# Optimization experiments

Hardware: AMD Instinct MI355X
Metric: run time of the kernel (lower is better)

Reference implementation:

```python
import jax, jax.numpy as jnp
import numpy as np

HEADS = 7
DIM_HEAD = 64
SCALE = DIM_HEAD ** -0.5


def setup_inputs() -> dict:
    key = jax.random.key(0)
    ks = jax.random.split(key, 6)
    b, n, dim = 8, 1024, 448
    inner = HEADS * DIM_HEAD  # 448
    x = jax.random.normal(ks[0], (b, n, dim), dtype=jnp.float32)
    w_qv = jax.random.normal(ks[1], (dim, 2 * inner), dtype=jnp.float32) * 0.02
    ext_k = jax.random.normal(ks[2], (HEADS, n, DIM_HEAD), dtype=jnp.float32)
    ext_bias = jax.random.normal(ks[3], (HEADS, n, n), dtype=jnp.float32)
    w_out = jax.random.normal(ks[4], (inner, dim), dtype=jnp.float32) * 0.02
    b_out = jnp.zeros((dim,), dtype=jnp.float32)
    return {"x": x, "w_qv": w_qv, "ext_k": ext_k, "ext_bias": ext_bias,
            "w_out": w_out, "b_out": b_out}


def reference(x, w_qv, ext_k, ext_bias, w_out, b_out):
    b, n, dim = x.shape
    qv = x @ w_qv                                   # [b, n, 2*inner]
    q, v = jnp.split(qv, 2, axis=-1)
    # b n (h d) -> b h n d
    q = q.reshape(b, n, HEADS, DIM_HEAD).transpose(0, 2, 1, 3)
    v = v.reshape(b, n, HEADS, DIM_HEAD).transpose(0, 2, 1, 3)
    # scores vs external learned key, additive bias applied BEFORE scale
    dots = (jnp.einsum('bhnd,hmd->bhnm', q, ext_k) + ext_bias[None]) * SCALE
    attn = jax.nn.softmax(dots, axis=-1)
    out = jnp.einsum('bhnm,bhmd->bhnd', attn, v)
    out = out.transpose(0, 2, 1, 3).reshape(b, n, HEADS * DIM_HEAD)
    return out @ w_out + b_out  # dropout is identity in eval mode
```

## Files before the change

kernel.cpp:

```cpp
#include <hip/hip_runtime.h>
#include <hip/hip_bf16.h>
#include <hip/hip_fp16.h>

#define BATCH 8
#define NSEQ 1024
#define DIMM 448
#define NHEAD 7
#define HDIM 64
#define MROWS (BATCH*NSEQ)
#define KDIM 448
#define SCALE_F 0.125f

typedef short short8 __attribute__((ext_vector_type(8)));
typedef float floatx16 __attribute__((ext_vector_type(16)));

#define MFMA32(a,b,c) __builtin_amdgcn_mfma_f32_32x32x16_bf16(a,b,c,0,0,0)

__device__ __forceinline__ unsigned short f2bf(float f){
    __hip_bfloat16 h = __float2bfloat16(f);
    return *reinterpret_cast<unsigned short*>(&h);
}
__device__ __forceinline__ float bf2f(unsigned short u){
    __hip_bfloat16 h; *reinterpret_cast<unsigned short*>(&h) = u;
    return __bfloat162float(h);
}
__device__ __forceinline__ float h2f(unsigned short u){
    __half h; *reinterpret_cast<unsigned short*>(&h) = u;
    return __half2float(h);
}
__device__ __forceinline__ unsigned short f2h(float f){
    __half h = __float2half(f);
    return *reinterpret_cast<unsigned short*>(&h);
}

__global__ __launch_bounds__(256)
void prep_all(const float* __restrict__ x, const float* __restrict__ ek,
              const float* __restrict__ wqv, const float* __restrict__ wout,
              const float* __restrict__ eb,
              unsigned short* __restrict__ xh, unsigned short* __restrict__ ekh,
              unsigned short* __restrict__ wqvTh, unsigned short* __restrict__ woTh,
              unsigned short* __restrict__ woTl, unsigned short* __restrict__ bp)
{
    __shared__ float T[2][64][33];
    const int bx = blockIdx.x, tid = threadIdx.x;

    if (bx < 3584) {
        int i = bx*256 + tid;
        float4 v = ((const float4*)x)[i];
        ((ushort4*)xh)[i] = make_ushort4(f2bf(v.x), f2bf(v.y), f2bf(v.z), f2bf(v.w));
    } else if (bx < 4032) {
        int i = (bx-3584)*256 + tid;
        float4 v = ((const float4*)ek)[i];
        ((ushort4*)ekh)[i] = make_ushort4(f2bf(v.x), f2bf(v.y), f2bf(v.z), f2bf(v.w));
    } else if (bx < 4228) {
        int lid = (bx-4032)*4 + (tid>>6);
        int kc = lid % 56, ng = lid / 56;
        int n = ng*64 + (tid&63);
        unsigned short h[8];
#pragma unroll
        for (int j = 0; j < 8; ++j) h[j] = f2bf(wqv[(size_t)(kc*8+j)*896 + n]);
        size_t o = (size_t)n*KDIM + kc*8;
        *(ushort4*)(wqvTh + o)     = make_ushort4(h[0],h[1],h[2],h[3]);
        *(ushort4*)(wqvTh + o + 4) = make_ushort4(h[4],h[5],h[6],h[7]);
    } else if (bx < 4340) {
        int lid = (bx-4228)*4 + (tid>>6);
        int kc = lid % 56, ng = lid / 56;
        int n = ng*64 + (tid&63);
        ushort4 h0={0,0,0,0}, h1={0,0,0,0}, l0={0,0,0,0}, l1={0,0,0,0};
        if (n < DIMM) {
            unsigned short h[8], l[8];
#pragma unroll
            for (int j = 0; j < 8; ++j) {
                float f = wout[(size_t)(kc*8+j)*DIMM + n];
                h[j] = f2bf(f); l[j] = f2bf(f - bf2f(h[j]));
            }
            h0 = make_ushort4(h[0],h[1],h[2],h[3]); h1 = make_ushort4(h[4],h[5],h[6],h[7]);
            l0 = make_ushort4(l[0],l[1],l[2],l[3]); l1 = make_ushort4(l[4],l[5],l[6],l[7]);
        }
        size_t o = (size_t)n*KDIM + kc*8;
        *(ushort4*)(woTh + o) = h0; *(ushort4*)(woTh + o + 4) = h1;
        *(ushort4*)(woTl + o) = l0; *(ushort4*)(woTl + o + 4) = l1;
    } else {
        const int sub = tid >> 7, st = tid & 127;
        const int lid = (bx-4340)*2 + sub;
        const int mt = lid & 31, qt = (lid>>5) & 15, h = lid >> 9;
#pragma unroll
        for (int it = 0; it < 4; ++it) {
            int idx = it*128 + st;
            int row = idx >> 3, c4 = (idx & 7)*4;
            float4 v = *(const float4*)(eb + ((size_t)(h*NSEQ + qt*64 + row))*NSEQ + mt*32 + c4);
            T[sub][row][c4+0]=v.x; T[sub][row][c4+1]=v.y;
            T[sub][row][c4+2]=v.z; T[sub][row][c4+3]=v.w;
        }
        __syncthreads();
        const int g2 = st >> 6, lane = st & 63;
        const int lq = lane & 31, quad = lane >> 5;
        const int q = g2*32 + lq;
        unsigned short* dst = bp + ((((size_t)h*16 + qt)*32 + mt)*4 + g2*2)*512 + lane*8;
#pragma unroll
        for (int jj = 0; jj < 2; ++jj) {
            unsigned short o[8];
#pragma unroll
            for (int t = 0; t < 8; ++t) {
                int m = (t&3) + 8*(t>>2) + 16*jj + 4*quad;
                o[t] = f2h(T[sub][q][m] * SCALE_F);
            }
            *(ushort4*)(dst + jj*512)     = make_ushort4(o[0],o[1],o[2],o[3]);
            *(ushort4*)(dst + jj*512 + 4) = make_ushort4(o[4],o[5],o[6],o[7]);
        }
    }
}

__global__ __launch_bounds__(256, 2)
void gemm1_grp(const unsigned short* __restrict__ Ah, const unsigned short* __restrict__ Bh,
               unsigned short* __restrict__ qd, unsigned short* __restrict__ vTd)
{
    const int tid = threadIdx.x;
    const int w = tid >> 6, lane = tid & 63;
    const int lq = lane & 31, lh = lane >> 5;
    const int m0 = (blockIdx.x*4 + w) * 64;
    const int y  = blockIdx.y;
    const int n0 = y * 64;
    const unsigned short* aB = Ah + (size_t)(m0 + lq)*KDIM + lh*8;
    const unsigned short* bB = Bh + (size_t)(n0 + lq)*KDIM + lh*8;

    floatx16 acc[2][2] = {};
    short8 aR[2][2][2], bR[2][2][2];
#define LD1(kt, par) {                                                        \
    _Pragma("unroll") for (int fm = 0; fm < 2; ++fm)                          \
    _Pragma("unroll") for (int c = 0; c < 2; ++c) {                           \
        aR[par][fm][c] = *(const short8*)(aB + (size_t)fm*32*KDIM + (kt)*32 + c*16); \
        bR[par][fm][c] = *(const short8*)(bB + (size_t)fm*32*KDIM + (kt)*32 + c*16); } }

    LD1(0, 0)
#pragma unroll
    for (int kt = 0; kt < 14; ++kt) {
        const int par = kt & 1;
        if (kt < 13) LD1(kt+1, par^1)
#pragma unroll
        for (int c = 0; c < 2; ++c)
#pragma unroll
            for (int fm = 0; fm < 2; ++fm)
#pragma unroll
                for (int fn = 0; fn < 2; ++fn)
                    acc[fm][fn] = MFMA32(aR[par][fm][c], bR[par][fn][c], acc[fm][fn]);
    }
#undef LD1

    if (y < NHEAD) {
#pragma unroll
        for (int fm = 0; fm < 2; ++fm)
#pragma unroll
            for (int fn = 0; fn < 2; ++fn) {
                const int d = fn*32 + lq;
#pragma unroll
                for (int r = 0; r < 16; ++r) {
                    const int gm = m0 + fm*32 + (r&3) + 8*(r>>2) + 4*lh;
                    const int b = gm >> 10, ns = gm & 1023;
                    qd[((size_t)((b*NHEAD + y)*NSEQ + ns))*HDIM + d] = f2bf(acc[fm][fn][r]);
                }
            }
    } else {
        const int head = y - NHEAD;
#pragma unroll
        for (int fm = 0; fm < 2; ++fm)
#pragma unroll
            for (int fn = 0; fn < 2; ++fn) {
                const int d = fn*32 + lq;
#pragma unroll
                for (int r = 0; r < 16; ++r) {
                    const int gm = m0 + fm*32 + (r&3) + 8*(r>>2) + 4*lh;
                    const int b = gm >> 10, ns = gm & 1023;
                    vTd[((size_t)((b*NHEAD + head)*HDIM + d))*NSEQ + ns] = f2bf(acc[fm][fn][r]);
                }
            }
    }
}

__global__ __launch_bounds__(256, 2)
void attn7s(const unsigned short* __restrict__ qh_g, const unsigned short* __restrict__ vTh,
            const unsigned short* __restrict__ ekh, const unsigned short* __restrict__ bp,
            unsigned short* __restrict__ aoh, unsigned short* __restrict__ aol)
{
    __shared__ unsigned short pS[4][1024];
    __shared__ float linv[4][2][32];

    const int tid = threadIdx.x;
    const int w = tid >> 6, lane = tid & 63;
    const int lq = lane & 31, lh = lane >> 5;

    const int orig = blockIdx.x;
    const int wg = (orig & 7)*28 + (orig >> 3);
    const int bq = wg & 1, qt = (wg >> 1) & 15, head = wg >> 5;
    const int b = bq*4 + w;
    const int bh = b*NHEAD + head;

    short8 qf[2][4];
#pragma unroll
    for (int g2 = 0; g2 < 2; ++g2)
#pragma unroll
        for (int c = 0; c < 4; ++c)
            qf[g2][c] = *(const short8*)(qh_g +
                ((size_t)(bh*NSEQ) + qt*64 + g2*32 + lq)*HDIM + c*16 + lh*8);

    const unsigned short* kB = ekh + ((size_t)head*NSEQ + lq)*HDIM + lh*8;
    const unsigned short* vB = vTh + ((size_t)(bh*HDIM) + lq)*NSEQ;
    const unsigned short* bB = bp + ((size_t)(head*16 + qt))*65536 + lane*8;

    short8 kR[2][4], vR[2][4], bR[2][4];
#define PREF(J, par) { const int mm = ((J) < 32) ? (J) : 0;                    \
    _Pragma("unroll") for (int c = 0; c < 4; ++c)                              \
        kR[par][c] = *(const short8*)(kB + (size_t)mm*2048 + c*16);            \
    _Pragma("unroll") for (int c2 = 0; c2 < 2; ++c2)                           \
    _Pragma("unroll") for (int h2 = 0; h2 < 2; ++h2)                           \
        vR[par][c2*2+h2] = *(const short8*)(vB + (size_t)(h2*32)*NSEQ + mm*32 + (c2*2+lh)*8); \
    _Pragma("unroll") for (int u = 0; u < 4; ++u)                              \
        bR[par][u] = *(const short8*)(bB + ((size_t)mm*4 + u)*512); }

    floatx16 O[2][2] = {};
    float ls[2] = {0.f, 0.f};

#define SEC(J, par, nxt) {                                                     \
    PREF((J)+1, nxt)                                                           \
    _Pragma("unroll") for (int g2 = 0; g2 < 2; ++g2) {                         \
        floatx16 S = {};                                                       \
        __builtin_amdgcn_s_setprio(1);                                         \
        _Pragma("unroll") for (int c = 0; c < 4; ++c)                          \
            S = MFMA32(kR[par][c], qf[g2][c], S);                              \
        __builtin_amdgcn_s_setprio(0);                                         \
        _Pragma("unroll") for (int g = 0; g < 4; ++g) {                        \
            unsigned short hb[4];                                              \
            _Pragma("unroll") for (int j2 = 0; j2 < 4; ++j2) {                 \
                const int i = g*4 + j2;                                        \
                float bs = h2f((unsigned short)bR[par][g2*2 + (i>>3)][i&7]);   \
                float pv = __expf(fmaf(S[i], SCALE_F, bs));                    \
                ls[g2] += pv;  hb[j2] = f2bf(pv);                              \
            }                                                                  \
            *(ushort4*)(pS[w] + g*256 + lq*8 + lh*4) = make_ushort4(hb[0],hb[1],hb[2],hb[3]); \
        }                                                                      \
        __builtin_amdgcn_s_setprio(1);                                         \
        _Pragma("unroll") for (int c2 = 0; c2 < 2; ++c2) {                     \
            short8 pf = *(const short8*)(pS[w] + ((c2*2+lh)*32 + lq)*8);       \
            O[g2][0] = MFMA32(pf, vR[par][c2*2+0], O[g2][0]);                  \
            O[g2][1] = MFMA32(pf, vR[par][c2*2+1], O[g2][1]);                  \
        }                                                                      \
        __builtin_amdgcn_s_setprio(0);                                         \
    } }

    PREF(0, 0)
    for (int jj = 0; jj < 16; ++jj) {
        SEC(2*jj,   0, 1)
        SEC(2*jj+1, 1, 0)
    }
#undef SEC
#undef PREF

    float lt0 = ls[0] + __shfl_xor(ls[0], 32);
    float lt1 = ls[1] + __shfl_xor(ls[1], 32);
    if (lh == 0) { linv[w][0][lq] = 1.f/lt0; linv[w][1][lq] = 1.f/lt1; }

#pragma unroll
    for (int g2 = 0; g2 < 2; ++g2)
#pragma unroll
        for (int r = 0; r < 16; ++r) {
            const int qr = (r&3) + 8*(r>>2) + 4*lh;
            const float inv = linv[w][g2][qr];
            const size_t o = ((size_t)(b*NSEQ) + qt*64 + g2*32 + qr)*DIMM + head*HDIM + lq;
            float v0 = O[g2][0][r]*inv, v1 = O[g2][1][r]*inv;
            unsigned short h0 = f2bf(v0), h1 = f2bf(v1);
            aoh[o]      = h0;  aol[o]      = f2bf(v0 - bf2f(h0));
            aoh[o + 32] = h1;  aol[o + 32] = f2bf(v1 - bf2f(h1));
        }
}

__global__ __launch_bounds__(128, 2)
void gemm2_grp(const unsigned short* __restrict__ Ah, const unsigned short* __restrict__ Al,
               const unsigned short* __restrict__ Bh, const unsigned short* __restrict__ Bl,
               const float* __restrict__ bias, float* __restrict__ out)
{
    const int tid = threadIdx.x;
    const int w = tid >> 6, lane = tid & 63;
    const int lq = lane & 31, lh = lane >> 5;
    const int m0 = (blockIdx.x*2 + w) * 64;
    const int n0 = blockIdx.y * 64;
    const unsigned short* aBh = Ah + (size_t)(m0 + lq)*KDIM + lh*8;
    const unsigned short* aBl = Al + (size_t)(m0 + lq)*KDIM + lh*8;
    const unsigned short* bBh = Bh + (size_t)(n0 + lq)*KDIM + lh*8;
    const unsigned short* bBl = Bl + (size_t)(n0 + lq)*KDIM + lh*8;

    floatx16 acc[2][2] = {};
    short8 aH[2][2][2], aL[2][2][2], bH[2][2][2], bL[2][2][2];
#define LD2(kt, par) {                                                        \
    _Pragma("unroll") for (int fm = 0; fm < 2; ++fm)                          \
    _Pragma("unroll") for (int c = 0; c < 2; ++c) {                           \
        const size_t off = (size_t)fm*32*KDIM + (kt)*32 + c*16;               \
        aH[par][fm][c] = *(const short8*)(aBh + off);                         \
        aL[par][fm][c] = *(const short8*)(aBl + off);                         \
        bH[par][fm][c] = *(const short8*)(bBh + off);                         \
        bL[par][fm][c] = *(const short8*)(bBl + off); } }

    LD2(0, 0)
#pragma unroll
    for (int kt = 0; kt < 14; ++kt) {
        const int par = kt & 1;
        if (kt < 13) LD2(kt+1, par^1)
#pragma unroll
        for (int c = 0; c < 2; ++c)
#pragma unroll
            for (int fm = 0; fm < 2; ++fm)
#pragma unroll
                for (int fn = 0; fn < 2; ++fn) {
                    acc[fm][fn] = MFMA32(aH[par][fm][c], bH[par][fn][c], acc[fm][fn]);
                    acc[fm][fn] = MFMA32(aL[par][fm][c], bH[par][fn][c], acc[fm][fn]);
                    acc[fm][fn] = MFMA32(aH[par][fm][c], bL[par][fn][c], acc[fm][fn]);
                }
    }
#undef LD2

#pragma unroll
    for (int fm = 0; fm < 2; ++fm)
#pragma unroll
        for (int fn = 0; fn < 2; ++fn) {
            const int gn = n0 + fn*32 + lq;
            const float bv = bias[gn];
#pragma unroll
            for (int r = 0; r < 16; ++r) {
                const int gm = m0 + fm*32 + (r&3) + 8*(r>>2) + 4*lh;
                out[(size_t)gm*DIMM + gn] = acc[fm][fn][r] + bv;
            }
        }
}

extern "C" void kernel_launch(void* const* d_in, const int* in_sizes, int n_in,
                              void* d_out, int out_size, void* d_ws, size_t ws_size,
                              hipStream_t stream)
{
    const float* x    = (const float*)d_in[0];
    const float* wqv  = (const float*)d_in[1];
    const float* ek   = (const float*)d_in[2];
    const float* eb   = (const float*)d_in[3];
    const float* wout = (const float*)d_in[4];
    const float* bout = (const float*)d_in[5];
    float* out = (float*)d_out;

    const size_t MK = (size_t)MROWS*KDIM;
    const size_t EK = (size_t)NHEAD*NSEQ*HDIM;
    unsigned short* p = (unsigned short*)d_ws;
    unsigned short* xh    = p;  p += MK;
    unsigned short* wqvTh = p;  p += (size_t)896*KDIM;
    unsigned short* woTh  = p;  p += (size_t)512*KDIM;
    unsigned short* woTl  = p;  p += (size_t)512*KDIM;
    unsigned short* ekh   = p;  p += EK;
    unsigned short* qh    = p;  p += MK;
    unsigned short* vTh   = p;  p += MK;
    unsigned short* bp    = p;  p += (size_t)NHEAD*NSEQ*NSEQ;
    unsigned short* aoh   = p;  p += MK;
    unsigned short* aol   = p;  p += MK;

    prep_all<<<6132, 256, 0, stream>>>(x, ek, wqv, wout, eb,
                                       xh, ekh, wqvTh, woTh, woTl, bp);
    gemm1_grp<<<dim3(32, 14), 256, 0, stream>>>(xh, wqvTh, qh, vTh);
    attn7s<<<224, 256, 0, stream>>>(qh, vTh, ekh, bp, aoh, aol);
    gemm2_grp<<<dim3(64, 7), 128, 0, stream>>>(aoh, aol, woTh, woTl, bout, out);
}
```

Baseline: 199.8 us.

## Pre-swizzle ext_k and V into MFMA fragment order for contiguous loads

```diff
diff --git a/kernel.cpp b/kernel.cpp
--- a/kernel.cpp
+++ b/kernel.cpp
@@ -50,7 +50,11 @@
         ((ushort4*)xh)[i] = make_ushort4(f2bf(v.x), f2bf(v.y), f2bf(v.z), f2bf(v.w));
     } else if (bx < 4032) {
         int i = (bx-3584)*256 + tid;
-        float4 v = ((const float4*)ek)[i];
+        const int h  = i >> 14, mm = (i >> 9) & 31, c = (i >> 7) & 3;
+        const int ln = (i >> 1) & 63, jh = i & 1;
+        const float* src = ek + ((size_t)(h*NSEQ) + mm*32 + (ln & 31))*HDIM
+                              + c*16 + (ln >> 5)*8 + jh*4;
+        float4 v = *(const float4*)src;
         ((ushort4*)ekh)[i] = make_ushort4(f2bf(v.x), f2bf(v.y), f2bf(v.z), f2bf(v.w));
     } else if (bx < 4228) {
         int lid = (bx-4032)*4 + (tid>>6);
@@ -163,22 +167,26 @@
     } else {
         const int head = y - NHEAD;
 #pragma unroll
-        for (int fm = 0; fm < 2; ++fm)
-#pragma unroll
-            for (int fn = 0; fn < 2; ++fn) {
-                const int d = fn*32 + lq;
-#pragma unroll
-                for (int r = 0; r < 16; ++r) {
-                    const int gm = m0 + fm*32 + (r&3) + 8*(r>>2) + 4*lh;
-                    const int b = gm >> 10, ns = gm & 1023;
-                    vTd[((size_t)((b*NHEAD + head)*HDIM + d))*NSEQ + ns] = f2bf(acc[fm][fn][r]);
+        for (int fm = 0; fm < 2; ++fm) {
+            const int gm0 = m0 + fm*32;
+            const int b = gm0 >> 10, mm = (gm0 & 1023) >> 5;
+            unsigned short* base = vTd + ((size_t)((b*NHEAD + head)*32 + mm))*2048;
+#pragma unroll
+            for (int fn = 0; fn < 2; ++fn)
+#pragma unroll
+                for (int rq = 0; rq < 4; ++rq) {
+                    const int u = (rq>>1)*2 + fn;
+                    const int lanep = (rq&1)*32 + lq;
+                    *(ushort4*)(base + u*512 + lanep*8 + 4*lh) = make_ushort4(
+                        f2bf(acc[fm][fn][rq*4+0]), f2bf(acc[fm][fn][rq*4+1]),
+                        f2bf(acc[fm][fn][rq*4+2]), f2bf(acc[fm][fn][rq*4+3]));
                 }
-            }
+        }
     }
 }
 
 __global__ __launch_bounds__(256, 2)
-void attn7s(const unsigned short* __restrict__ qh_g, const unsigned short* __restrict__ vTh,
+void attn7p(const unsigned short* __restrict__ qh_g, const unsigned short* __restrict__ vTh,
             const unsigned short* __restrict__ ekh, const unsigned short* __restrict__ bp,
             unsigned short* __restrict__ aoh, unsigned short* __restrict__ aol)
 {
@@ -203,19 +211,18 @@
             qf[g2][c] = *(const short8*)(qh_g +
                 ((size_t)(bh*NSEQ) + qt*64 + g2*32 + lq)*HDIM + c*16 + lh*8);
 
-    const unsigned short* kB = ekh + ((size_t)head*NSEQ + lq)*HDIM + lh*8;
-    const unsigned short* vB = vTh + ((size_t)(bh*HDIM) + lq)*NSEQ;
+    const unsigned short* kB = ekh + (size_t)head*65536 + lane*8;
+    const unsigned short* vB = vTh + (size_t)bh*65536 + lane*8;
     const unsigned short* bB = bp + ((size_t)(head*16 + qt))*65536 + lane*8;
 
     short8 kR[2][4], vR[2][4], bR[2][4];
 #define PREF(J, par) { const int mm = ((J) < 32) ? (J) : 0;                    \
     _Pragma("unroll") for (int c = 0; c < 4; ++c)                              \
-        kR[par][c] = *(const short8*)(kB + (size_t)mm*2048 + c*16);            \
-    _Pragma("unroll") for (int c2 = 0; c2 < 2; ++c2)                           \
-    _Pragma("unroll") for (int h2 = 0; h2 < 2; ++h2)                           \
-        vR[par][c2*2+h2] = *(const short8*)(vB + (size_t)(h2*32)*NSEQ + mm*32 + (c2*2+lh)*8); \
+        kR[par][c] = *(const short8*)(kB + (size_t)mm*2048 + c*512);           \
     _Pragma("unroll") for (int u = 0; u < 4; ++u)                              \
-        bR[par][u] = *(const short8*)(bB + ((size_t)mm*4 + u)*512); }
+        vR[par][u] = *(const short8*)(vB + (size_t)mm*2048 + u*512);           \
+    _Pragma("unroll") for (int u = 0; u < 4; ++u)                              \
+        bR[par][u] = *(const short8*)(bB + (size_t)mm*2048 + u*512); }
 
     floatx16 O[2][2] = {};
     float ls[2] = {0.f, 0.f};
@@ -224,10 +231,8 @@
     PREF((J)+1, nxt)                                                           \
     _Pragma("unroll") for (int g2 = 0; g2 < 2; ++g2) {                         \
         floatx16 S = {};                                                       \
-        __builtin_amdgcn_s_setprio(1);                                         \
         _Pragma("unroll") for (int c = 0; c < 4; ++c)                          \
             S = MFMA32(kR[par][c], qf[g2][c], S);                              \
-        __builtin_amdgcn_s_setprio(0);                                         \
         _Pragma("unroll") for (int g = 0; g < 4; ++g) {                        \
             unsigned short hb[4];                                              \
             _Pragma("unroll") for (int j2 = 0; j2 < 4; ++j2) {                 \
@@ -238,14 +243,11 @@
             }                                                                  \
             *(ushort4*)(pS[w] + g*256 + lq*8 + lh*4) = make_ushort4(hb[0],hb[1],hb[2],hb[3]); \
         }                                                                      \
-        __builtin_amdgcn_s_setprio(1);                                         \
         _Pragma("unroll") for (int c2 = 0; c2 < 2; ++c2) {                     \
             short8 pf = *(const short8*)(pS[w] + ((c2*2+lh)*32 + lq)*8);       \
             O[g2][0] = MFMA32(pf, vR[par][c2*2+0], O[g2][0]);                  \
             O[g2][1] = MFMA32(pf, vR[par][c2*2+1], O[g2][1]);                  \
-        }                                                                      \
-        __builtin_amdgcn_s_setprio(0);                                         \
-    } }
+        } } }
 
     PREF(0, 0)
     for (int jj = 0; jj < 16; ++jj) {
@@ -360,6 +362,6 @@
     prep_all<<<6132, 256, 0, stream>>>(x, ek, wqv, wout, eb,
                                        xh, ekh, wqvTh, woTh, woTl, bp);
     gemm1_grp<<<dim3(32, 14), 256, 0, stream>>>(xh, wqvTh, qh, vTh);
-    attn7s<<<224, 256, 0, stream>>>(qh, vTh, ekh, bp, aoh, aol);
+    attn7p<<<224, 256, 0, stream>>>(qh, vTh, ekh, bp, aoh, aol);
     gemm2_grp<<<dim3(64, 7), 128, 0, stream>>>(aoh, aol, woTh, woTl, bout, out);
 }
```

Measured after the change: 186.0 us. 1.07x faster.
